# Optimization experiments

Hardware: AMD Instinct MI355X
Metric: run time of the kernel (lower is better)

## Reference

```python
import jax, jax.numpy as jnp
import numpy as np

D_MODEL = 1024
NUM_HEADS = 16
D_K = D_MODEL // NUM_HEADS


def setup_inputs() -> dict:
    key = jax.random.key(0)
    ks = jax.random.split(key, 9)
    B, S = 4, 2048
    scale = 1.0 / np.sqrt(D_MODEL)
    x = jax.random.normal(ks[0], (B, S, D_MODEL), dtype=jnp.float32)
    Wq = jax.random.uniform(ks[1], (D_MODEL, D_MODEL), jnp.float32, -scale, scale)
    Wk = jax.random.uniform(ks[2], (D_MODEL, D_MODEL), jnp.float32, -scale, scale)
    Wv = jax.random.uniform(ks[3], (D_MODEL, D_MODEL), jnp.float32, -scale, scale)
    Wo = jax.random.uniform(ks[4], (D_MODEL, D_MODEL), jnp.float32, -scale, scale)
    bq = jax.random.uniform(ks[5], (D_MODEL,), jnp.float32, -scale, scale)
    bk = jax.random.uniform(ks[6], (D_MODEL,), jnp.float32, -scale, scale)
    bv = jax.random.uniform(ks[7], (D_MODEL,), jnp.float32, -scale, scale)
    bo = jax.random.uniform(ks[8], (D_MODEL,), jnp.float32, -scale, scale)
    return {"x": x, "Wq": Wq, "bq": bq, "Wk": Wk, "bk": bk, "Wv": Wv, "bv": bv, "Wo": Wo, "bo": bo}


def _split_heads(t, B, S):
    # (B, S, D) -> (B, H, S, d_k)
    return t.reshape(B, S, NUM_HEADS, D_K).transpose(0, 2, 1, 3)


def reference(x, Wq, bq, Wk, bk, Wv, bv, Wo, bo):
    B, S, D = x.shape
    Q = _split_heads(x @ Wq + bq, B, S)
    K = _split_heads(x @ Wk + bk, B, S)
    V = _split_heads(x @ Wv + bv, B, S)
    # scores: (B, H, S, S) — naive materialization, faithful to original
    scores = jnp.einsum('bhqd,bhkd->bhqk', Q, K) / np.sqrt(D_K)
    weights = jax.nn.softmax(scores.astype(jnp.float32), axis=-1).astype(scores.dtype)
    # dropout p=0.0 in eval mode -> identity
    attn = jnp.einsum('bhqk,bhkd->bhqd', weights, V)
    attn = attn.transpose(0, 2, 1, 3).reshape(B, S, D)
    return attn @ Wo + bo
```

## Files before the change

### kernel.cpp

```cpp
#include <hip/hip_runtime.h>
#include <hip/hip_bf16.h>
#include <stdint.h>
#include <string.h>

using u16 = unsigned short;
typedef __attribute__((ext_vector_type(8))) short short8;
typedef __attribute__((ext_vector_type(4))) float f32x4;

__device__ __forceinline__ u16 f2bf(float f) {
  union { float f; unsigned int u; } x; x.f = f;
  unsigned int u = x.u;
  return (u16)((u + 0x7fffu + ((u >> 16) & 1u)) >> 16);
}
__device__ __forceinline__ unsigned int pk_bf16(float a, float b) {
  float2 t; t.x = a; t.y = b;
  __hip_bfloat162 h = __float22bfloat162_rn(t);
  unsigned int u; memcpy(&u, &h, 4);
  return u;
}
__device__ __forceinline__ void gl_lds16(const u16* g, u16* l) {
  __builtin_amdgcn_global_load_lds((const __attribute__((address_space(1))) void*)g,
                                   (__attribute__((address_space(3))) void*)l, 16, 0, 0);
}

__device__ __forceinline__ void pl_swap(unsigned int& a, unsigned int& b) {
  auto r1 = __builtin_amdgcn_permlane32_swap(a, b, false, false);
  auto r2 = __builtin_amdgcn_permlane16_swap(r1[0], r1[1], false, false);
  a = r2[0]; b = r2[1];
}

#define SCALE_LOG2E 0.18033688011112042f

__global__ void __launch_bounds__(256) conv_x(
    const float* __restrict__ in, u16* __restrict__ out, int n4) {
  const int t = blockIdx.x * 256 + threadIdx.x;
  if (t >= n4) return;
  const float4 v = ((const float4*)in)[t];
  uint2 o;
  o.x = pk_bf16(v.x, v.y);
  o.y = pk_bf16(v.z, v.w);
  ((uint2*)out)[t] = o;
}

__global__ void __launch_bounds__(256) transpose_w(
    const float* __restrict__ W0, const float* __restrict__ W1,
    const float* __restrict__ W2, const float* __restrict__ W3,
    u16* __restrict__ Wt) {
  __shared__ alignas(16) u16 t[64][65];
  const int z = blockIdx.z;
  const float* in = (z == 0) ? W0 : (z == 1) ? W1 : (z == 2) ? W2 : W3;
  u16* out = Wt + (size_t)z * 1024 * 1024;
  const int tx = threadIdx.x & 63, ty = threadIdx.x >> 6;
  const int r0 = blockIdx.y * 64, c0 = blockIdx.x * 64;
#pragma unroll
  for (int rr = ty; rr < 64; rr += 4) t[rr][tx] = f2bf(in[(size_t)(r0 + rr) * 1024 + c0 + tx]);
  __syncthreads();
#pragma unroll
  for (int rr = ty; rr < 64; rr += 4) out[(size_t)(c0 + rr) * 1024 + r0 + tx] = t[tx][rr];
}

__device__ __forceinline__ void gemm_core(
    const u16* __restrict__ A, const u16* __restrict__ Bt,
    u16* As, u16* Bs, int m0, int n0, int K, f32x4 (&acc)[4][4]) {
  const int tid = threadIdx.x;
  const int wave = tid >> 6, lane = tid & 63;
  const int quad = lane >> 4, l16 = lane & 15;
  const int wr = wave >> 1, wc = wave & 1;
  const int lr8 = lane >> 3;
  const int cbg = ((lane & 7) ^ lr8) * 8;
  const int sw = (l16 & 7);
  for (int k0 = 0; k0 < K; k0 += 64) {
    __syncthreads();
#pragma unroll
    for (int u = 0; u < 4; ++u) {
      gl_lds16(A  + (size_t)(m0 + u * 32 + wave * 8 + lr8) * K + k0 + cbg,
               &As[u * 2048 + wave * 512]);
      gl_lds16(Bt + (size_t)(n0 + u * 32 + wave * 8 + lr8) * K + k0 + cbg,
               &Bs[u * 2048 + wave * 512]);
    }
    __syncthreads();
#pragma unroll
    for (int ks = 0; ks < 2; ++ks) {
      const int kc = ((ks * 4 + quad) ^ sw) * 8;
      short8 af[4], bfr[4];
#pragma unroll
      for (int i = 0; i < 4; ++i)
        af[i] = *(const short8*)&As[(wr * 64 + i * 16 + l16) * 64 + kc];
#pragma unroll
      for (int j = 0; j < 4; ++j)
        bfr[j] = *(const short8*)&Bs[(wc * 64 + j * 16 + l16) * 64 + kc];
#pragma unroll
      for (int i = 0; i < 4; ++i)
#pragma unroll
        for (int j = 0; j < 4; ++j)
          acc[i][j] = __builtin_amdgcn_mfma_f32_16x16x32_bf16(af[i], bfr[j], acc[i][j], 0, 0, 0);
    }
  }
}

__global__ void __launch_bounds__(256) gemm_qkv(
    const u16* __restrict__ A, const u16* __restrict__ Wt,
    const float* __restrict__ bq, const float* __restrict__ bk, const float* __restrict__ bv,
    u16* __restrict__ Qb, u16* __restrict__ Kb, u16* __restrict__ Vtb) {
  __shared__ alignas(16) u16 As[128 * 64];
  __shared__ alignas(16) u16 Bs[128 * 64];
  const int tsel = blockIdx.x >> 3;
  const int n0 = (blockIdx.x & 7) * 128;
  const int m0 = blockIdx.y * 128;
  const u16* Bt = Wt + (size_t)tsel * 1048576;
  const float* bias = (tsel == 0) ? bq : (tsel == 1) ? bk : bv;

  f32x4 acc[4][4];
#pragma unroll
  for (int i = 0; i < 4; ++i)
#pragma unroll
    for (int j = 0; j < 4; ++j) acc[i][j] = (f32x4){0.f, 0.f, 0.f, 0.f};

  gemm_core(A, Bt, As, Bs, m0, n0, 1024, acc);

  const int tid = threadIdx.x;
  const int wave = tid >> 6, lane = tid & 63;
  const int quad = lane >> 4, l16 = lane & 15;
  const int wr = wave >> 1, wc = wave & 1;

  if (tsel < 2) {
    u16* C = tsel ? Kb : Qb;
    const float scl = tsel ? 1.0f : SCALE_LOG2E;
#pragma unroll
    for (int j = 0; j < 4; ++j) {
      const int n = n0 + wc * 64 + j * 16 + l16;
      const float bvf = bias[n];
      const int h = n >> 6, d = n & 63;
#pragma unroll
      for (int i = 0; i < 4; ++i) {
        const int mbase = m0 + wr * 64 + i * 16 + quad * 4;
#pragma unroll
        for (int r = 0; r < 4; ++r) {
          const int m = mbase + r;
          const int b = m >> 11, s = m & 2047;
          C[((((size_t)b * 16 + h) * 2048) + s) * 64 + d] = f2bf((acc[i][j][r] + bvf) * scl);
        }
      }
    }
  } else {
#pragma unroll
    for (int j = 0; j < 4; ++j) {
      const int n = n0 + wc * 64 + j * 16 + l16;
      const float bvf = bias[n];
      const int h = n >> 6, d = n & 63;
#pragma unroll
      for (int i = 0; i < 4; ++i) {
        const int mbase = m0 + wr * 64 + i * 16 + quad * 4;
        const int b = mbase >> 11, s = mbase & 2047;
        uint2 o;
        o.x = pk_bf16(acc[i][j][0] + bvf, acc[i][j][1] + bvf);
        o.y = pk_bf16(acc[i][j][2] + bvf, acc[i][j][3] + bvf);
        *(uint2*)&Vtb[(((size_t)b * 16 + h) * 64 + d) * 2048 + s] = o;
      }
    }
  }
}

__global__ void __launch_bounds__(256) gemm_out(
    const u16* __restrict__ A, const u16* __restrict__ Bt,
    const float* __restrict__ bias, float* __restrict__ C, int N) {
  __shared__ alignas(16) u16 As[128 * 64];
  __shared__ alignas(16) u16 Bs[128 * 64];
  const int m0 = blockIdx.y * 128;
  const int n0 = blockIdx.x * 128;
  f32x4 acc[4][4];
#pragma unroll
  for (int i = 0; i < 4; ++i)
#pragma unroll
    for (int j = 0; j < 4; ++j) acc[i][j] = (f32x4){0.f, 0.f, 0.f, 0.f};

  gemm_core(A, Bt, As, Bs, m0, n0, 1024, acc);

  const int tid = threadIdx.x;
  const int wave = tid >> 6, lane = tid & 63;
  const int quad = lane >> 4, l16 = lane & 15;
  const int wr = wave >> 1, wc = wave & 1;
#pragma unroll
  for (int j = 0; j < 4; ++j) {
    const int n = n0 + wc * 64 + j * 16 + l16;
    const float bvf = bias[n];
#pragma unroll
    for (int i = 0; i < 4; ++i) {
      const int mbase = m0 + wr * 64 + i * 16 + quad * 4;
#pragma unroll
      for (int r = 0; r < 4; ++r)
        C[(size_t)(mbase + r) * N + n] = acc[i][j][r] + bvf;
    }
  }
}

__global__ void __launch_bounds__(256) flash_attn(
    const u16* __restrict__ Q, const u16* __restrict__ Kp,
    const u16* __restrict__ Vt, u16* __restrict__ Aout) {
  __shared__ alignas(16) u16 Qs[128 * 64];
  __shared__ alignas(16) u16 Ks[2][64 * 64];
  __shared__ alignas(16) u16 Vs[2][64 * 64];

  const int tid = threadIdx.x;
  const int wave = tid >> 6;
  const int lane = tid & 63;
  const int quad = lane >> 4;
  const int l16 = lane & 15;

  const int i = blockIdx.x;
  const int bh = (i & 7) * 8 + (i >> 7);
  const int q0 = ((i >> 3) & 15) * 128;
  const int b = bh >> 4, h = bh & 15;

  const u16* Qg = Q + (size_t)bh * 2048 * 64;
  const u16* Kg = Kp + (size_t)bh * 2048 * 64;
  const u16* Vg = Vt + (size_t)bh * 64 * 2048;

  const int lr8 = lane >> 3;
  const int cbg = ((lane & 7) ^ lr8) * 8;

#pragma unroll
  for (int t = 0; t < 4; ++t) {
    const int c = wave * 4 + t;
    gl_lds16(Qg + (size_t)(q0 + c * 8 + lr8) * 64 + cbg, &Qs[c * 8 * 64]);
  }
  {
#pragma unroll
    for (int t = 0; t < 2; ++t) {
      const int c = wave * 2 + t;
      gl_lds16(Kg + (size_t)(c * 8 + lr8) * 64 + cbg, &Ks[0][c * 8 * 64]);
      gl_lds16(Vg + (size_t)(c * 8 + lr8) * 2048 + cbg, &Vs[0][c * 8 * 64]);
    }
  }

  f32x4 oacc[2][4];
#pragma unroll
  for (int qb = 0; qb < 2; ++qb)
#pragma unroll
    for (int t = 0; t < 4; ++t) oacc[qb][t] = (f32x4){0.f, 0.f, 0.f, 0.f};
  f32x4 lacc[2];
  lacc[0] = (f32x4){0.f, 0.f, 0.f, 0.f};
  lacc[1] = (f32x4){0.f, 0.f, 0.f, 0.f};
  const int sw = (l16 & 7) * 8;

  short8 ones;
#pragma unroll
  for (int i2 = 0; i2 < 8; ++i2) ones[i2] = (short)0x3F80;

  __syncthreads();
  short8 qf[2][2];
#pragma unroll
  for (int qb = 0; qb < 2; ++qb)
#pragma unroll
    for (int ks = 0; ks < 2; ++ks)
      qf[qb][ks] = *(const short8*)&Qs[(wave * 32 + qb * 16 + l16) * 64 + (((ks * 4 + quad) * 8) ^ sw)];

  for (int kt = 0; kt < 32; ++kt) {
    const int p = kt & 1;
    if (kt + 1 < 32) {
      const int s1 = (kt + 1) * 64;
#pragma unroll
      for (int t = 0; t < 2; ++t) {
        const int c = wave * 2 + t;
        gl_lds16(Kg + (size_t)(s1 + c * 8 + lr8) * 64 + cbg, &Ks[p ^ 1][c * 8 * 64]);
        gl_lds16(Vg + (size_t)(c * 8 + lr8) * 2048 + s1 + cbg, &Vs[p ^ 1][c * 8 * 64]);
      }
    }
    const u16* Kc = &Ks[p][0];
    const u16* Vc = &Vs[p][0];

    f32x4 sacc[2][4];
#pragma unroll
    for (int qb = 0; qb < 2; ++qb)
#pragma unroll
      for (int t = 0; t < 4; ++t) sacc[qb][t] = (f32x4){0.f, 0.f, 0.f, 0.f};
#pragma unroll
    for (int ks = 0; ks < 2; ++ks) {
#pragma unroll
      for (int t = 0; t < 4; ++t) {
        const short8 akf = *(const short8*)&Kc[(t * 16 + l16) * 64 + (((ks * 4 + quad) * 8) ^ sw)];
#pragma unroll
        for (int qb = 0; qb < 2; ++qb)
          sacc[qb][t] = __builtin_amdgcn_mfma_f32_16x16x32_bf16(akf, qf[qb][ks], sacc[qb][t], 0, 0, 0);
      }
    }

    short8 bpf[2][2];
#pragma unroll
    for (int qb = 0; qb < 2; ++qb) {
      unsigned int w[4][2];
#pragma unroll
      for (int t = 0; t < 4; ++t) {
        const float p0 = __builtin_amdgcn_exp2f(sacc[qb][t][0]);
        const float p1 = __builtin_amdgcn_exp2f(sacc[qb][t][1]);
        const float p2 = __builtin_amdgcn_exp2f(sacc[qb][t][2]);
        const float p3 = __builtin_amdgcn_exp2f(sacc[qb][t][3]);
        w[t][0] = pk_bf16(p0, p1);
        w[t][1] = pk_bf16(p2, p3);
      }
      pl_swap(w[0][0], w[1][0]);
      pl_swap(w[0][1], w[1][1]);
      pl_swap(w[2][0], w[3][0]);
      pl_swap(w[2][1], w[3][1]);
      union { short8 s8; unsigned int u[4]; } pb;
      pb.u[0] = w[0][0]; pb.u[1] = w[0][1]; pb.u[2] = w[1][0]; pb.u[3] = w[1][1];
      bpf[qb][0] = pb.s8;
      pb.u[0] = w[2][0]; pb.u[1] = w[2][1]; pb.u[2] = w[3][0]; pb.u[3] = w[3][1];
      bpf[qb][1] = pb.s8;
    }

#pragma unroll
    for (int s = 0; s < 2; ++s)
#pragma unroll
      for (int qb = 0; qb < 2; ++qb)
        lacc[qb] = __builtin_amdgcn_mfma_f32_16x16x32_bf16(ones, bpf[qb][s], lacc[qb], 0, 0, 0);

#pragma unroll
    for (int s = 0; s < 2; ++s) {
#pragma unroll
      for (int t = 0; t < 4; ++t) {
        const short8 avf = *(const short8*)&Vc[(t * 16 + l16) * 64 + (((s * 4 + quad) * 8) ^ sw)];
#pragma unroll
        for (int qb = 0; qb < 2; ++qb)
          oacc[qb][t] = __builtin_amdgcn_mfma_f32_16x16x32_bf16(avf, bpf[qb][s], oacc[qb][t], 0, 0, 0);
      }
    }

    __syncthreads();
  }

#pragma unroll
  for (int qb = 0; qb < 2; ++qb) {
    const float inv = 1.0f / lacc[qb][0];
    const int qrow = q0 + wave * 32 + qb * 16 + l16;
    const size_t base = ((size_t)b * 2048 + qrow) * 1024 + h * 64 + quad * 4;
#pragma unroll
    for (int t = 0; t < 4; ++t) {
      uint2 o;
      o.x = pk_bf16(oacc[qb][t][0] * inv, oacc[qb][t][1] * inv);
      o.y = pk_bf16(oacc[qb][t][2] * inv, oacc[qb][t][3] * inv);
      *(uint2*)&Aout[base + t * 16] = o;
    }
  }
}

extern "C" void kernel_launch(void* const* d_in, const int* in_sizes, int n_in,
                              void* d_out, int out_size, void* d_ws, size_t ws_size,
                              hipStream_t stream) {
  (void)in_sizes; (void)n_in; (void)out_size; (void)ws_size;
  const float* x  = (const float*)d_in[0];
  const float* Wq = (const float*)d_in[1];
  const float* bq = (const float*)d_in[2];
  const float* Wk = (const float*)d_in[3];
  const float* bk = (const float*)d_in[4];
  const float* Wv = (const float*)d_in[5];
  const float* bv = (const float*)d_in[6];
  const float* Wo = (const float*)d_in[7];
  const float* bo = (const float*)d_in[8];
  float* out = (float*)d_out;

  u16* ws = (u16*)d_ws;
  const size_t SZ = (size_t)4 * 16 * 2048 * 64;
  u16* xb   = ws;
  u16* Qb   = ws + SZ;
  u16* Kb   = ws + 2 * SZ;
  u16* Vtb  = ws + 3 * SZ;
  u16* Wt   = ws + 4 * SZ;
  u16* Attn = ws;

  conv_x<<<dim3(8192), dim3(256), 0, stream>>>(x, xb, 2097152);
  transpose_w<<<dim3(16, 16, 4), dim3(256), 0, stream>>>(Wq, Wk, Wv, Wo, Wt);
  gemm_qkv<<<dim3(24, 64), dim3(256), 0, stream>>>(xb, Wt, bq, bk, bv, Qb, Kb, Vtb);
  flash_attn<<<dim3(1024), dim3(256), 0, stream>>>(Qb, Kb, Vtb, Attn);
  gemm_out<<<dim3(8, 64), dim3(256), 0, stream>>>(Attn, Wt + (size_t)3 * 1048576, bo, out, 1024);
}
```

Baseline: 308.9 us.

## Double-buffer GEMM LDS tiles and remap blocks for XCD-local L2 reuse

```diff
diff --git a/kernel.cpp b/kernel.cpp
--- a/kernel.cpp
+++ b/kernel.cpp
@@ -61,7 +61,8 @@
 
 __device__ __forceinline__ void gemm_core(
     const u16* __restrict__ A, const u16* __restrict__ Bt,
-    u16* As, u16* Bs, int m0, int n0, int K, f32x4 (&acc)[4][4]) {
+    u16 (*As)[8192], u16 (*Bs)[8192],
+    int m0, int n0, int K, f32x4 (&acc)[4][4]) {
   const int tid = threadIdx.x;
   const int wave = tid >> 6, lane = tid & 63;
   const int quad = lane >> 4, l16 = lane & 15;
@@ -69,32 +70,48 @@
   const int lr8 = lane >> 3;
   const int cbg = ((lane & 7) ^ lr8) * 8;
   const int sw = (l16 & 7);
-  for (int k0 = 0; k0 < K; k0 += 64) {
-    __syncthreads();
-#pragma unroll
-    for (int u = 0; u < 4; ++u) {
-      gl_lds16(A  + (size_t)(m0 + u * 32 + wave * 8 + lr8) * K + k0 + cbg,
-               &As[u * 2048 + wave * 512]);
-      gl_lds16(Bt + (size_t)(n0 + u * 32 + wave * 8 + lr8) * K + k0 + cbg,
-               &Bs[u * 2048 + wave * 512]);
-    }
-    __syncthreads();
+  const int NT = K >> 6;
+
+#pragma unroll
+  for (int u = 0; u < 4; ++u) {
+    gl_lds16(A  + (size_t)(m0 + u * 32 + wave * 8 + lr8) * K + cbg,
+             &As[0][u * 2048 + wave * 512]);
+    gl_lds16(Bt + (size_t)(n0 + u * 32 + wave * 8 + lr8) * K + cbg,
+             &Bs[0][u * 2048 + wave * 512]);
+  }
+  __syncthreads();
+
+  for (int t = 0; t < NT; ++t) {
+    const int p = t & 1;
+    if (t + 1 < NT) {
+      const int k1 = (t + 1) * 64;
+#pragma unroll
+      for (int u = 0; u < 4; ++u) {
+        gl_lds16(A  + (size_t)(m0 + u * 32 + wave * 8 + lr8) * K + k1 + cbg,
+                 &As[p ^ 1][u * 2048 + wave * 512]);
+        gl_lds16(Bt + (size_t)(n0 + u * 32 + wave * 8 + lr8) * K + k1 + cbg,
+                 &Bs[p ^ 1][u * 2048 + wave * 512]);
+      }
+    }
+    const u16* Ap = As[p];
+    const u16* Bp = Bs[p];
 #pragma unroll
     for (int ks = 0; ks < 2; ++ks) {
       const int kc = ((ks * 4 + quad) ^ sw) * 8;
       short8 af[4], bfr[4];
 #pragma unroll
       for (int i = 0; i < 4; ++i)
-        af[i] = *(const short8*)&As[(wr * 64 + i * 16 + l16) * 64 + kc];
+        af[i] = *(const short8*)&Ap[(wr * 64 + i * 16 + l16) * 64 + kc];
 #pragma unroll
       for (int j = 0; j < 4; ++j)
-        bfr[j] = *(const short8*)&Bs[(wc * 64 + j * 16 + l16) * 64 + kc];
+        bfr[j] = *(const short8*)&Bp[(wc * 64 + j * 16 + l16) * 64 + kc];
 #pragma unroll
       for (int i = 0; i < 4; ++i)
 #pragma unroll
         for (int j = 0; j < 4; ++j)
           acc[i][j] = __builtin_amdgcn_mfma_f32_16x16x32_bf16(af[i], bfr[j], acc[i][j], 0, 0, 0);
     }
+    __syncthreads();
   }
 }
 
@@ -102,19 +119,21 @@
     const u16* __restrict__ A, const u16* __restrict__ Wt,
     const float* __restrict__ bq, const float* __restrict__ bk, const float* __restrict__ bv,
     u16* __restrict__ Qb, u16* __restrict__ Kb, u16* __restrict__ Vtb) {
-  __shared__ alignas(16) u16 As[128 * 64];
-  __shared__ alignas(16) u16 Bs[128 * 64];
-  const int tsel = blockIdx.x >> 3;
-  const int n0 = (blockIdx.x & 7) * 128;
-  const int m0 = blockIdx.y * 128;
+  __shared__ alignas(16) u16 As[2][8192];
+  __shared__ alignas(16) u16 Bs[2][8192];
+  const int i = blockIdx.x;
+  const int xcd = i & 7, j = i >> 3;
+  const int tsel = j >> 6, r = j & 63;
+  const int n0 = (r & 7) * 128;
+  const int m0 = ((r >> 3) * 8 + xcd) * 128;
   const u16* Bt = Wt + (size_t)tsel * 1048576;
   const float* bias = (tsel == 0) ? bq : (tsel == 1) ? bk : bv;
 
   f32x4 acc[4][4];
 #pragma unroll
-  for (int i = 0; i < 4; ++i)
-#pragma unroll
-    for (int j = 0; j < 4; ++j) acc[i][j] = (f32x4){0.f, 0.f, 0.f, 0.f};
+  for (int ii = 0; ii < 4; ++ii)
+#pragma unroll
+    for (int jj = 0; jj < 4; ++jj) acc[ii][jj] = (f32x4){0.f, 0.f, 0.f, 0.f};
 
   gemm_core(A, Bt, As, Bs, m0, n0, 1024, acc);
 
@@ -127,34 +146,34 @@
     u16* C = tsel ? Kb : Qb;
     const float scl = tsel ? 1.0f : SCALE_LOG2E;
 #pragma unroll
-    for (int j = 0; j < 4; ++j) {
-      const int n = n0 + wc * 64 + j * 16 + l16;
+    for (int jj = 0; jj < 4; ++jj) {
+      const int n = n0 + wc * 64 + jj * 16 + l16;
       const float bvf = bias[n];
       const int h = n >> 6, d = n & 63;
 #pragma unroll
-      for (int i = 0; i < 4; ++i) {
-        const int mbase = m0 + wr * 64 + i * 16 + quad * 4;
-#pragma unroll
-        for (int r = 0; r < 4; ++r) {
-          const int m = mbase + r;
+      for (int ii = 0; ii < 4; ++ii) {
+        const int mbase = m0 + wr * 64 + ii * 16 + quad * 4;
+#pragma unroll
+        for (int rr = 0; rr < 4; ++rr) {
+          const int m = mbase + rr;
           const int b = m >> 11, s = m & 2047;
-          C[((((size_t)b * 16 + h) * 2048) + s) * 64 + d] = f2bf((acc[i][j][r] + bvf) * scl);
+          C[((((size_t)b * 16 + h) * 2048) + s) * 64 + d] = f2bf((acc[ii][jj][rr] + bvf) * scl);
         }
       }
     }
   } else {
 #pragma unroll
-    for (int j = 0; j < 4; ++j) {
-      const int n = n0 + wc * 64 + j * 16 + l16;
+    for (int jj = 0; jj < 4; ++jj) {
+      const int n = n0 + wc * 64 + jj * 16 + l16;
       const float bvf = bias[n];
       const int h = n >> 6, d = n & 63;
 #pragma unroll
-      for (int i = 0; i < 4; ++i) {
-        const int mbase = m0 + wr * 64 + i * 16 + quad * 4;
+      for (int ii = 0; ii < 4; ++ii) {
+        const int mbase = m0 + wr * 64 + ii * 16 + quad * 4;
         const int b = mbase >> 11, s = mbase & 2047;
         uint2 o;
-        o.x = pk_bf16(acc[i][j][0] + bvf, acc[i][j][1] + bvf);
-        o.y = pk_bf16(acc[i][j][2] + bvf, acc[i][j][3] + bvf);
+        o.x = pk_bf16(acc[ii][jj][0] + bvf, acc[ii][jj][1] + bvf);
+        o.y = pk_bf16(acc[ii][jj][2] + bvf, acc[ii][jj][3] + bvf);
         *(uint2*)&Vtb[(((size_t)b * 16 + h) * 64 + d) * 2048 + s] = o;
       }
     }
@@ -164,15 +183,17 @@
 __global__ void __launch_bounds__(256) gemm_out(
     const u16* __restrict__ A, const u16* __restrict__ Bt,
     const float* __restrict__ bias, float* __restrict__ C, int N) {
-  __shared__ alignas(16) u16 As[128 * 64];
-  __shared__ alignas(16) u16 Bs[128 * 64];
-  const int m0 = blockIdx.y * 128;
-  const int n0 = blockIdx.x * 128;
+  __shared__ alignas(16) u16 As[2][8192];
+  __shared__ alignas(16) u16 Bs[2][8192];
+  const int i = blockIdx.x;
+  const int xcd = i & 7, j = i >> 3;
+  const int n0 = (j & 7) * 128;
+  const int m0 = ((j >> 3) * 8 + xcd) * 128;
   f32x4 acc[4][4];
 #pragma unroll
-  for (int i = 0; i < 4; ++i)
-#pragma unroll
-    for (int j = 0; j < 4; ++j) acc[i][j] = (f32x4){0.f, 0.f, 0.f, 0.f};
+  for (int ii = 0; ii < 4; ++ii)
+#pragma unroll
+    for (int jj = 0; jj < 4; ++jj) acc[ii][jj] = (f32x4){0.f, 0.f, 0.f, 0.f};
 
   gemm_core(A, Bt, As, Bs, m0, n0, 1024, acc);
 
@@ -181,15 +202,15 @@
   const int quad = lane >> 4, l16 = lane & 15;
   const int wr = wave >> 1, wc = wave & 1;
 #pragma unroll
-  for (int j = 0; j < 4; ++j) {
-    const int n = n0 + wc * 64 + j * 16 + l16;
+  for (int jj = 0; jj < 4; ++jj) {
+    const int n = n0 + wc * 64 + jj * 16 + l16;
     const float bvf = bias[n];
 #pragma unroll
-    for (int i = 0; i < 4; ++i) {
-      const int mbase = m0 + wr * 64 + i * 16 + quad * 4;
-#pragma unroll
-      for (int r = 0; r < 4; ++r)
-        C[(size_t)(mbase + r) * N + n] = acc[i][j][r] + bvf;
+    for (int ii = 0; ii < 4; ++ii) {
+      const int mbase = m0 + wr * 64 + ii * 16 + quad * 4;
+#pragma unroll
+      for (int rr = 0; rr < 4; ++rr)
+        C[(size_t)(mbase + rr) * N + n] = acc[ii][jj][rr] + bvf;
     }
   }
 }
@@ -370,7 +391,7 @@
 
   conv_x<<<dim3(8192), dim3(256), 0, stream>>>(x, xb, 2097152);
   transpose_w<<<dim3(16, 16, 4), dim3(256), 0, stream>>>(Wq, Wk, Wv, Wo, Wt);
-  gemm_qkv<<<dim3(24, 64), dim3(256), 0, stream>>>(xb, Wt, bq, bk, bv, Qb, Kb, Vtb);
+  gemm_qkv<<<dim3(1536), dim3(256), 0, stream>>>(xb, Wt, bq, bk, bv, Qb, Kb, Vtb);
   flash_attn<<<dim3(1024), dim3(256), 0, stream>>>(Qb, Kb, Vtb, Attn);
-  gemm_out<<<dim3(8, 64), dim3(256), 0, stream>>>(Attn, Wt + (size_t)3 * 1048576, bo, out, 1024);
-}
+  gemm_out<<<dim3(512), dim3(256), 0, stream>>>(Attn, Wt + (size_t)3 * 1048576, bo, out, 1024);
+}
```

Result: slower. 320.8 us (+3.8%).
